# Kernel optimization log

Measured on AMD Instinct MI355X. Metric: run time of the kernel, lower is better.

Reference implementation:

```python
import jax, jax.numpy as jnp
import numpy as np


def make_base_grid(D, H, W, dtype):
    # torch.affine_grid(align_corners=True) base coords: last dim is (x, y, z)
    # where x varies along W, y along H, z along D, each in [-1, 1].
    zs = jnp.linspace(-1.0, 1.0, D, dtype=dtype)
    ys = jnp.linspace(-1.0, 1.0, H, dtype=dtype)
    xs = jnp.linspace(-1.0, 1.0, W, dtype=dtype)
    gz, gy, gx = jnp.meshgrid(zs, ys, xs, indexing='ij')  # each (D,H,W)
    return jnp.stack([gx, gy, gz], axis=-1)  # (D,H,W,3)


def trilinear_sample(vol, grid):
    # vol: (C,D,H,W); grid: (D,H,W,3) normalized coords (x,y,z);
    # align_corners=True, padding_mode='zeros' (torch grid_sample defaults).
    C, D, H, W = vol.shape
    ix = (grid[..., 0] + 1.0) * 0.5 * (W - 1)
    iy = (grid[..., 1] + 1.0) * 0.5 * (H - 1)
    iz = (grid[..., 2] + 1.0) * 0.5 * (D - 1)
    ix0f, iy0f, iz0f = jnp.floor(ix), jnp.floor(iy), jnp.floor(iz)
    wx, wy, wz = ix - ix0f, iy - iy0f, iz - iz0f
    ix0, iy0, iz0 = ix0f.astype(jnp.int32), iy0f.astype(jnp.int32), iz0f.astype(jnp.int32)
    ix1, iy1, iz1 = ix0 + 1, iy0 + 1, iz0 + 1

    def corner(zi, yi, xi, w):
        valid = ((zi >= 0) & (zi < D) & (yi >= 0) & (yi < H) & (xi >= 0) & (xi < W))
        zc = jnp.clip(zi, 0, D - 1)
        yc = jnp.clip(yi, 0, H - 1)
        xc = jnp.clip(xi, 0, W - 1)
        v = vol[:, zc, yc, xc]  # (C,D,H,W)
        return v * (w * valid.astype(vol.dtype))[None]

    one = jnp.asarray(1.0, vol.dtype)
    out = (corner(iz0, iy0, ix0, (one - wz) * (one - wy) * (one - wx))
           + corner(iz0, iy0, ix1, (one - wz) * (one - wy) * wx)
           + corner(iz0, iy1, ix0, (one - wz) * wy * (one - wx))
           + corner(iz0, iy1, ix1, (one - wz) * wy * wx)
           + corner(iz1, iy0, ix0, wz * (one - wy) * (one - wx))
           + corner(iz1, iy0, ix1, wz * (one - wy) * wx)
           + corner(iz1, iy1, ix0, wz * wy * (one - wx))
           + corner(iz1, iy1, ix1, wz * wy * wx))
    return out  # (C,D,H,W)


def setup_inputs() -> dict:
    key = jax.random.key(0)
    kx, ky = jax.random.split(key)
    shape = (1, 1, 192, 192, 192)
    x = jax.random.uniform(kx, shape, dtype=jnp.float32)
    y = jax.random.uniform(ky, shape, dtype=jnp.float32)
    return {"x": x, "y": y}


def reference(x, y):
    N, C, D, H, W = x.shape
    base = make_base_grid(D, H, W, x.dtype)  # (D,H,W,3) == identity affine_grid
    xv = x[:, 0]  # (N,D,H,W), channel 0 only as in the torch code
    yv = y[:, 0]
    x_sum = jnp.sum(x)
    y_sum = jnp.sum(y)
    # weighted center of mass for each normalized coordinate (x,y,z)
    cm_x = jnp.einsum('ndhw,dhwk->k', xv, base) / x_sum  # (3,)
    cm_y = jnp.einsum('ndhw,dhwk->k', yv, base) / y_sum  # (3,)
    t = cm_x - cm_y  # translation placed in theta[:, :, 3]
    grid = base + t  # (D,H,W,3): affine_grid with identity + translation
    grid_b = jnp.broadcast_to(grid[None], (N, D, H, W, 3))
    transformed = jax.vmap(trilinear_sample)(x, grid_b)  # (N,C,D,H,W)
    return transformed, grid_b
```

## Files before the change

### kernel.cpp

```cpp
#include <hip/hip_runtime.h>
#include <math.h>

#define DD 192
#define HH 192
#define WW 192
#define NVOX (DD*HH*WW)
#define NV4  (NVOX/4)
#define RB   1024
#define RT   256

struct Consts {
    float tx, ty, tz;
    float wgt[8];
    int   dx0, dy0, dz0;
};

__device__ __forceinline__ float gcoord(int i, int n) {
    return -1.0f + (float)i * (2.0f / (float)(n - 1));
}

__global__ void reduce_kernel(const float* __restrict__ x,
                              const float* __restrict__ y,
                              double* __restrict__ partials) {
    double acc[8] = {0,0,0,0,0,0,0,0};
    int tid = blockIdx.x * blockDim.x + threadIdx.x;
    const float4* x4 = (const float4*)x;
    const float4* y4 = (const float4*)y;
    for (int i = tid; i < NV4; i += RB * RT) {
        float4 xv = x4[i];
        float4 yv = y4[i];
        int base = i * 4;
        int w = base % WW;
        int rem = base / WW;
        int h = rem % HH;
        int d = rem / HH;
        float gy = gcoord(h, HH);
        float gz = gcoord(d, DD);
        float xs[4] = {xv.x, xv.y, xv.z, xv.w};
        float ys[4] = {yv.x, yv.y, yv.z, yv.w};
        #pragma unroll
        for (int k = 0; k < 4; ++k) {
            float gx = gcoord(w + k, WW);
            acc[0] += (double)xs[k];
            acc[1] += (double)(xs[k] * gx);
            acc[2] += (double)(xs[k] * gy);
            acc[3] += (double)(xs[k] * gz);
            acc[4] += (double)ys[k];
            acc[5] += (double)(ys[k] * gx);
            acc[6] += (double)(ys[k] * gy);
            acc[7] += (double)(ys[k] * gz);
        }
    }
    #pragma unroll
    for (int q = 0; q < 8; ++q) {
        double v = acc[q];
        #pragma unroll
        for (int off = 32; off > 0; off >>= 1)
            v += __shfl_down(v, off, 64);
        acc[q] = v;
    }
    __shared__ double lds[4][8];
    int lane = threadIdx.x & 63;
    int wave = threadIdx.x >> 6;
    if (lane == 0) {
        #pragma unroll
        for (int q = 0; q < 8; ++q) lds[wave][q] = acc[q];
    }
    __syncthreads();
    if (threadIdx.x < 8) {
        int q = threadIdx.x;
        partials[q * RB + blockIdx.x] = lds[0][q] + lds[1][q] + lds[2][q] + lds[3][q];
    }
}

__global__ void finalize_kernel(const double* __restrict__ partials,
                                Consts* __restrict__ cs) {
    double s[8];
    #pragma unroll
    for (int q = 0; q < 8; ++q) {
        double v = 0.0;
        for (int i = threadIdx.x; i < RB; i += 256) v += partials[q * RB + i];
        #pragma unroll
        for (int off = 32; off > 0; off >>= 1)
            v += __shfl_down(v, off, 64);
        s[q] = v;
    }
    __shared__ double lds[4][8];
    int lane = threadIdx.x & 63;
    int wave = threadIdx.x >> 6;
    if (lane == 0) {
        #pragma unroll
        for (int q = 0; q < 8; ++q) lds[wave][q] = s[q];
    }
    __syncthreads();
    if (threadIdx.x == 0) {
        double sums[8];
        #pragma unroll
        for (int q = 0; q < 8; ++q)
            sums[q] = lds[0][q] + lds[1][q] + lds[2][q] + lds[3][q];
        double tx = sums[1] / sums[0] - sums[5] / sums[4];
        double ty = sums[2] / sums[0] - sums[6] / sums[4];
        double tz = sums[3] / sums[0] - sums[7] / sums[4];
        cs->tx = (float)tx; cs->ty = (float)ty; cs->tz = (float)tz;
        double cx = tx * (double)(WW - 1) * 0.5;
        double cy = ty * (double)(HH - 1) * 0.5;
        double cz = tz * (double)(DD - 1) * 0.5;
        double fx = floor(cx), fy = floor(cy), fz = floor(cz);
        float wx = (float)(cx - fx), wy = (float)(cy - fy), wz = (float)(cz - fz);
        cs->dx0 = (int)fx; cs->dy0 = (int)fy; cs->dz0 = (int)fz;
        #pragma unroll
        for (int k = 0; k < 8; ++k) {
            float wzz = (k & 4) ? wz : 1.0f - wz;
            float wyy = (k & 2) ? wy : 1.0f - wy;
            float wxx = (k & 1) ? wx : 1.0f - wx;
            cs->wgt[k] = wzz * wyy * wxx;
        }
    }
}

__global__ void __launch_bounds__(256) main_kernel(const float* __restrict__ x,
                                                   const Consts* __restrict__ csp,
                                                   float* __restrict__ out_t,
                                                   float4* __restrict__ out_g4) {
    __shared__ float gbuf[768];
    const Consts c = *csp;
    int idx = blockIdx.x * 256 + threadIdx.x;
    int w = idx % WW;
    int rem = idx / WW;
    int h = rem % HH;
    int d = rem / HH;
    float gx = gcoord(w, WW) + c.tx;
    float gy = gcoord(h, HH) + c.ty;
    float gz = gcoord(d, DD) + c.tz;
    gbuf[3 * threadIdx.x + 0] = gx;
    gbuf[3 * threadIdx.x + 1] = gy;
    gbuf[3 * threadIdx.x + 2] = gz;
    __syncthreads();
    if (threadIdx.x < 192) {
        const float4* src = (const float4*)gbuf;
        out_g4[blockIdx.x * 192 + threadIdx.x] = src[threadIdx.x];
    }
    int xi0 = w + c.dx0, yi0 = h + c.dy0, zi0 = d + c.dz0;
    int xi1 = xi0 + 1,  yi1 = yi0 + 1,  zi1 = zi0 + 1;
    int xs0 = min(max(xi0, 0), WW - 1), xs1 = min(max(xi1, 0), WW - 1);
    int ys0 = min(max(yi0, 0), HH - 1), ys1 = min(max(yi1, 0), HH - 1);
    int zs0 = min(max(zi0, 0), DD - 1), zs1 = min(max(zi1, 0), DD - 1);
    float vx0 = ((unsigned)xi0 < (unsigned)WW) ? 1.0f : 0.0f;
    float vx1 = ((unsigned)xi1 < (unsigned)WW) ? 1.0f : 0.0f;
    float vy0 = ((unsigned)yi0 < (unsigned)HH) ? 1.0f : 0.0f;
    float vy1 = ((unsigned)yi1 < (unsigned)HH) ? 1.0f : 0.0f;
    float vz0 = ((unsigned)zi0 < (unsigned)DD) ? 1.0f : 0.0f;
    float vz1 = ((unsigned)zi1 < (unsigned)DD) ? 1.0f : 0.0f;
    int rb00 = (zs0 * HH + ys0) * WW;
    int rb01 = (zs0 * HH + ys1) * WW;
    int rb10 = (zs1 * HH + ys0) * WW;
    int rb11 = (zs1 * HH + ys1) * WW;
    float acc =
        x[rb00 + xs0] * (c.wgt[0] * (vz0 * vy0 * vx0)) +
        x[rb00 + xs1] * (c.wgt[1] * (vz0 * vy0 * vx1)) +
        x[rb01 + xs0] * (c.wgt[2] * (vz0 * vy1 * vx0)) +
        x[rb01 + xs1] * (c.wgt[3] * (vz0 * vy1 * vx1)) +
        x[rb10 + xs0] * (c.wgt[4] * (vz1 * vy0 * vx0)) +
        x[rb10 + xs1] * (c.wgt[5] * (vz1 * vy0 * vx1)) +
        x[rb11 + xs0] * (c.wgt[6] * (vz1 * vy1 * vx0)) +
        x[rb11 + xs1] * (c.wgt[7] * (vz1 * vy1 * vx1));
    out_t[idx] = acc;
}

extern "C" void kernel_launch(void* const* d_in, const int* in_sizes, int n_in,
                              void* d_out, int out_size, void* d_ws, size_t ws_size,
                              hipStream_t stream) {
    const float* x = (const float*)d_in[0];
    const float* y = (const float*)d_in[1];
    float* out = (float*)d_out;
    float* out_t = out;
    float4* out_g4 = (float4*)(out + NVOX);
    double* partials = (double*)d_ws;
    Consts* cs = (Consts*)((char*)d_ws + 8 * RB * sizeof(double));
    reduce_kernel<<<RB, RT, 0, stream>>>(x, y, partials);
    finalize_kernel<<<1, 256, 0, stream>>>(partials, cs);
    main_kernel<<<NVOX / 256, 256, 0, stream>>>(x, cs, out_t, out_g4);
}
```

Baseline: 174.7 us.

## Process four voxels per thread with vector loads and nontemporal stores

```diff
diff --git a/kernel.cpp b/kernel.cpp
--- a/kernel.cpp
+++ b/kernel.cpp
@@ -9,6 +9,8 @@
 #define RB   1024
 #define RT   256
 
+typedef float f32x4 __attribute__((ext_vector_type(4)));
+
 struct Consts {
     float tx, ty, tz;
     float wgt[8];
@@ -17,6 +19,12 @@
 
 __device__ __forceinline__ float gcoord(int i, int n) {
     return -1.0f + (float)i * (2.0f / (float)(n - 1));
+}
+
+__device__ __forceinline__ f32x4 load4u(const float* p) {
+    f32x4 v;
+    __builtin_memcpy(&v, p, sizeof(v));
+    return v;
 }
 
 __global__ void reduce_kernel(const float* __restrict__ x,
@@ -120,51 +128,76 @@
 
 __global__ void __launch_bounds__(256) main_kernel(const float* __restrict__ x,
                                                    const Consts* __restrict__ csp,
-                                                   float* __restrict__ out_t,
-                                                   float4* __restrict__ out_g4) {
-    __shared__ float gbuf[768];
+                                                   f32x4* __restrict__ out_t4,
+                                                   f32x4* __restrict__ out_g4) {
     const Consts c = *csp;
-    int idx = blockIdx.x * 256 + threadIdx.x;
-    int w = idx % WW;
-    int rem = idx / WW;
+    int t = blockIdx.x * 256 + threadIdx.x;
+    int vb = t * 4;
+    int w0 = vb % WW;
+    int rem = vb / WW;
     int h = rem % HH;
     int d = rem / HH;
-    float gx = gcoord(w, WW) + c.tx;
-    float gy = gcoord(h, HH) + c.ty;
-    float gz = gcoord(d, DD) + c.tz;
-    gbuf[3 * threadIdx.x + 0] = gx;
-    gbuf[3 * threadIdx.x + 1] = gy;
-    gbuf[3 * threadIdx.x + 2] = gz;
-    __syncthreads();
-    if (threadIdx.x < 192) {
-        const float4* src = (const float4*)gbuf;
-        out_g4[blockIdx.x * 192 + threadIdx.x] = src[threadIdx.x];
-    }
-    int xi0 = w + c.dx0, yi0 = h + c.dy0, zi0 = d + c.dz0;
-    int xi1 = xi0 + 1,  yi1 = yi0 + 1,  zi1 = zi0 + 1;
-    int xs0 = min(max(xi0, 0), WW - 1), xs1 = min(max(xi1, 0), WW - 1);
+
+    float gx0 = gcoord(w0 + 0, WW) + c.tx;
+    float gx1 = gcoord(w0 + 1, WW) + c.tx;
+    float gx2 = gcoord(w0 + 2, WW) + c.tx;
+    float gx3 = gcoord(w0 + 3, WW) + c.tx;
+    float gy  = gcoord(h, HH) + c.ty;
+    float gz  = gcoord(d, DD) + c.tz;
+    f32x4 f0 = {gx0, gy, gz, gx1};
+    f32x4 f1 = {gy, gz, gx2, gy};
+    f32x4 f2 = {gz, gx3, gy, gz};
+    __builtin_nontemporal_store(f0, &out_g4[3 * t + 0]);
+    __builtin_nontemporal_store(f1, &out_g4[3 * t + 1]);
+    __builtin_nontemporal_store(f2, &out_g4[3 * t + 2]);
+
+    int yi0 = h + c.dy0, yi1 = yi0 + 1;
+    int zi0 = d + c.dz0, zi1 = zi0 + 1;
     int ys0 = min(max(yi0, 0), HH - 1), ys1 = min(max(yi1, 0), HH - 1);
     int zs0 = min(max(zi0, 0), DD - 1), zs1 = min(max(zi1, 0), DD - 1);
-    float vx0 = ((unsigned)xi0 < (unsigned)WW) ? 1.0f : 0.0f;
-    float vx1 = ((unsigned)xi1 < (unsigned)WW) ? 1.0f : 0.0f;
     float vy0 = ((unsigned)yi0 < (unsigned)HH) ? 1.0f : 0.0f;
     float vy1 = ((unsigned)yi1 < (unsigned)HH) ? 1.0f : 0.0f;
     float vz0 = ((unsigned)zi0 < (unsigned)DD) ? 1.0f : 0.0f;
     float vz1 = ((unsigned)zi1 < (unsigned)DD) ? 1.0f : 0.0f;
-    int rb00 = (zs0 * HH + ys0) * WW;
-    int rb01 = (zs0 * HH + ys1) * WW;
-    int rb10 = (zs1 * HH + ys0) * WW;
-    int rb11 = (zs1 * HH + ys1) * WW;
-    float acc =
-        x[rb00 + xs0] * (c.wgt[0] * (vz0 * vy0 * vx0)) +
-        x[rb00 + xs1] * (c.wgt[1] * (vz0 * vy0 * vx1)) +
-        x[rb01 + xs0] * (c.wgt[2] * (vz0 * vy1 * vx0)) +
-        x[rb01 + xs1] * (c.wgt[3] * (vz0 * vy1 * vx1)) +
-        x[rb10 + xs0] * (c.wgt[4] * (vz1 * vy0 * vx0)) +
-        x[rb10 + xs1] * (c.wgt[5] * (vz1 * vy0 * vx1)) +
-        x[rb11 + xs0] * (c.wgt[6] * (vz1 * vy1 * vx0)) +
-        x[rb11 + xs1] * (c.wgt[7] * (vz1 * vy1 * vx1));
-    out_t[idx] = acc;
+    int   rb[4]  = { (zs0 * HH + ys0) * WW, (zs0 * HH + ys1) * WW,
+                     (zs1 * HH + ys0) * WW, (zs1 * HH + ys1) * WW };
+    float sr[4]  = { vz0 * vy0, vz0 * vy1, vz1 * vy0, vz1 * vy1 };
+
+    int xi0g = w0 + c.dx0;
+    f32x4 acc = {0.0f, 0.0f, 0.0f, 0.0f};
+
+    if (xi0g >= 0 && xi0g + 4 <= WW - 1) {
+        #pragma unroll
+        for (int r = 0; r < 4; ++r) {
+            float w0r = sr[r] * c.wgt[2 * r + 0];
+            float w1r = sr[r] * c.wgt[2 * r + 1];
+            const float* p = x + rb[r] + xi0g;
+            f32x4 v  = load4u(p);
+            float v4 = p[4];
+            acc.x += w0r * v.x + w1r * v.y;
+            acc.y += w0r * v.y + w1r * v.z;
+            acc.z += w0r * v.z + w1r * v.w;
+            acc.w += w0r * v.w + w1r * v4;
+        }
+    } else {
+        float res[4];
+        #pragma unroll
+        for (int k = 0; k < 4; ++k) {
+            int xi0 = xi0g + k, xi1 = xi0 + 1;
+            int xs0 = min(max(xi0, 0), WW - 1), xs1 = min(max(xi1, 0), WW - 1);
+            float vx0 = ((unsigned)xi0 < (unsigned)WW) ? 1.0f : 0.0f;
+            float vx1 = ((unsigned)xi1 < (unsigned)WW) ? 1.0f : 0.0f;
+            float a = 0.0f;
+            #pragma unroll
+            for (int r = 0; r < 4; ++r) {
+                a += x[rb[r] + xs0] * (sr[r] * c.wgt[2 * r + 0] * vx0);
+                a += x[rb[r] + xs1] * (sr[r] * c.wgt[2 * r + 1] * vx1);
+            }
+            res[k] = a;
+        }
+        acc.x = res[0]; acc.y = res[1]; acc.z = res[2]; acc.w = res[3];
+    }
+    __builtin_nontemporal_store(acc, &out_t4[t]);
 }
 
 extern "C" void kernel_launch(void* const* d_in, const int* in_sizes, int n_in,
@@ -173,11 +206,11 @@
     const float* x = (const float*)d_in[0];
     const float* y = (const float*)d_in[1];
     float* out = (float*)d_out;
-    float* out_t = out;
-    float4* out_g4 = (float4*)(out + NVOX);
+    f32x4* out_t4 = (f32x4*)out;
+    f32x4* out_g4 = (f32x4*)(out + NVOX);
     double* partials = (double*)d_ws;
     Consts* cs = (Consts*)((char*)d_ws + 8 * RB * sizeof(double));
     reduce_kernel<<<RB, RT, 0, stream>>>(x, y, partials);
     finalize_kernel<<<1, 256, 0, stream>>>(partials, cs);
-    main_kernel<<<NVOX / 256, 256, 0, stream>>>(x, cs, out_t, out_g4);
-}
+    main_kernel<<<NVOX / 4 / 256, 256, 0, stream>>>(x, cs, out_t4, out_g4);
+}
```

Result: slower. 228.2 us (+30.6%).
